# Performance work log

Measured on AMD Instinct MI355X. Metric: run time of the kernel, lower is better.

## Reference

```python
import math
import jax, jax.numpy as jnp
import numpy as np

CHUNK = 32
PROB_FLOOR = 0.02
EPS = 1e-5

def l2norm(x):
    return x * jax.lax.rsqrt(jnp.sum(x * x, -1, keepdims=True) + 1e-6)

def causal_dwconv(x, w):
    # x: (B, L, C), w: (C, K) depthwise causal FIR (left-padded)
    B, L, C = x.shape
    K = w.shape[-1]
    y = jax.lax.conv_general_dilated(jnp.transpose(x, (0, 2, 1)), w[:, None, :], (1,), [(K - 1, 0)], feature_group_count=C)
    return jnp.transpose(y, (0, 2, 1))

def delta_rule_chunkwise(q, k, v, beta, chunk=CHUNK):
    # q,k: (b,h,L,dk)  v: (b,h,L,dv)  beta: (b,h,L)
    b, h, L, dk = q.shape
    dv = v.shape[-1]
    pad = (-L) % chunk
    if pad:
        q = jnp.pad(q, ((0, 0), (0, 0), (0, pad), (0, 0)))
        k = jnp.pad(k, ((0, 0), (0, 0), (0, pad), (0, 0)))
        v = jnp.pad(v, ((0, 0), (0, 0), (0, pad), (0, 0)))
        beta = jnp.pad(beta, ((0, 0), (0, 0), (0, pad)))
    Lp = L + pad
    n = Lp // chunk
    q = l2norm(q)
    k = l2norm(k)
    v = v * beta[..., None]
    kb = k * beta[..., None]
    r = lambda t: t.reshape(b, h, n, chunk, t.shape[-1])
    q, k, v, kb = (r(q), r(k), r(v), r(kb))
    i_ = jnp.arange(chunk)
    strict_lower = (i_[:, None] > i_[None, :]).astype(q.dtype)
    lower_incl = (i_[:, None] >= i_[None, :]).astype(q.dtype)
    inv = -(kb @ jnp.swapaxes(k, -1, -2)) * strict_lower  # (b,h,n,c,c)
    for i in range(1, chunk):  # row-wise forward substitution; chunk is static so unrolled
        inv = inv.at[..., i, :].add(jnp.einsum('...j,...jk->...k', inv[..., i, :], inv))
    inv = inv + jnp.eye(chunk, dtype=q.dtype)
    u = inv @ v   # (b,h,n,c,dv)
    w = inv @ kb  # (b,h,n,c,dk)
    mv = lambda t: jnp.moveaxis(t, 2, 0)  # scan over chunks
    def step(S, xs):
        qi, ki, ui, wi = xs
        attn = (qi @ jnp.swapaxes(ki, -1, -2)) * lower_incl
        ui2 = ui - wi @ S
        oi = qi @ S + attn @ ui2
        return S + jnp.swapaxes(ki, -1, -2) @ ui2, oi
    S0 = jnp.zeros((b, h, dk, dv), q.dtype)
    S, outs = jax.lax.scan(step, S0, (mv(q), mv(k), mv(u), mv(w)))
    out = jnp.moveaxis(outs, 0, 2).reshape(b, h, Lp, dv)[:, :, :L]
    return out, S

def head_stats(x):
    # x: (B,L,H,D) -> (B,L,4): [mean, var, abs-mean, l2] per head, averaged over heads
    mean = x.mean(-1)
    var = ((x - mean[..., None]) ** 2).mean(-1)
    am = jnp.abs(x).mean(-1)
    l2 = jnp.sqrt((x * x).sum(-1))
    return jnp.stack([mean, var, am, l2], -1).mean(2)

def rmsnorm(x, w):
    return x * jax.lax.rsqrt((x * x).mean(-1, keepdims=True) + EPS) * w

def setup_inputs():
    key = jax.random.key(0)
    ks = jax.random.split(key, 20)
    B, L, D, H = 2, 4096, 1024, 4
    dv = D // H
    f32 = jnp.float32
    rn = lambda k, shape, s: (jax.random.normal(k, shape) * s).astype(f32)
    fir = lambda k, shape: rn(k, shape, 0.02).at[..., -1].add(1.0)  # near-identity causal filter
    return {
        'hidden_states': jax.random.normal(ks[0], (B, L, D), f32),
        'Wq': rn(ks[1], (D, D), 0.02), 'Wk': rn(ks[2], (D, D), 0.02), 'Wv': rn(ks[3], (D, D), 0.02),
        'Wb': rn(ks[4], (D, H), 0.02),
        'wq_conv': fir(ks[5], (D, 4)), 'wk_conv': fir(ks[6], (D, 4)), 'wv_conv': fir(ks[7], (D, 4)),
        'fir_long': fir(ks[8], (H, dv, 64)), 'fir_short': fir(ks[9], (H, dv, 5)),
        'Wg1': rn(ks[10], (D + 16, D), 0.02), 'bg1': jnp.zeros((D,), f32),
        'Wg2': rn(ks[11], (D, 4), 0.02), 'bg2': jnp.array([-0.5, -0.5, 1.0, 3.0], f32),
        'logit_temp': jnp.array([math.log(math.expm1(0.7))], f32),
        'conv_res_logit': jnp.full((H,), -1.0, f32),
        'Wres': rn(ks[12], (D, H), 0.02), 'bres': jnp.full((H,), -1.0, f32),
        'Wog1': rn(ks[13], (D + 8, D // 2), 0.02), 'bog1': jnp.zeros((D // 2,), f32),
        'Wog2': rn(ks[14], (D // 2, 1), 0.02), 'bog2': jnp.full((1,), -1.0986122886681098, f32),
        'norm_w': jnp.ones((dv,), f32),
        'Wo': rn(ks[15], (D, D), 0.02),
    }

def reference(hidden_states, Wq, Wk, Wv, Wb, wq_conv, wk_conv, wv_conv, fir_long, fir_short, Wg1, bg1, Wg2, bg2, logit_temp, conv_res_logit, Wres, bres, Wog1, bog1, Wog2, bog2, norm_w, Wo):
    B, L, D = hidden_states.shape
    H = Wb.shape[-1]
    silu = jax.nn.silu
    q_in = silu(causal_dwconv(hidden_states @ Wq, wq_conv))
    k_in = silu(causal_dwconv(hidden_states @ Wk, wk_conv))
    v_in = silu(causal_dwconv(hidden_states @ Wv, wv_conv))
    dk = q_in.shape[-1] // H
    dv = v_in.shape[-1] // H
    q = q_in.reshape(B, L, H, dk)
    k = k_in.reshape(B, L, H, dk)
    v_direct = v_in.reshape(B, L, H, dv)
    beta = jax.nn.sigmoid(hidden_states @ Wb)  # (B,L,H)
    do, S = delta_rule_chunkwise(jnp.transpose(q, (0, 2, 1, 3)), jnp.transpose(k, (0, 2, 1, 3)), jnp.transpose(v_direct, (0, 2, 1, 3)), jnp.transpose(beta, (0, 2, 1)))
    delta_out = jnp.transpose(do, (0, 2, 1, 3))  # (B,L,H,dv)
    local_long = causal_dwconv(v_in, fir_long.reshape(-1, fir_long.shape[-1])).reshape(B, L, H, dv)
    local_short = causal_dwconv(v_in, fir_short.reshape(-1, fir_short.shape[-1])).reshape(B, L, H, dv)
    stats = jnp.concatenate([head_stats(t) for t in (local_short, local_long, delta_out, v_direct)], -1)  # (B,L,16)
    gate_in = jnp.concatenate([hidden_states, stats], -1)
    logits = (jax.nn.gelu(gate_in @ Wg1 + bg1, approximate=False) @ Wg2 + bg2) / jax.nn.softplus(logit_temp)
    p = jax.nn.softmax(logits, -1)
    p = jnp.clip(p, PROB_FLOOR, None)
    p = p / p.sum(-1, keepdims=True)
    pw = p[:, :, None, :]  # (B,L,1,4)
    o = pw[..., 0:1] * local_short + pw[..., 1:2] * local_long + pw[..., 2:3] * delta_out + pw[..., 3:4] * v_direct
    res_gate = jax.nn.sigmoid(hidden_states @ Wres + bres)  # (B,L,H)
    static = jax.nn.sigmoid(conv_res_logit)  # (H,)
    o = o + (static[None, None, :] * res_gate)[..., None] * local_short
    og_stats = jnp.concatenate([head_stats(o), head_stats(v_direct)], -1)  # (B,L,8)
    og_in = jnp.concatenate([hidden_states, og_stats], -1)
    og = jax.nn.sigmoid(jax.nn.gelu(og_in @ Wog1 + bog1, approximate=False) @ Wog2 + bog2)  # (B,L,1)
    o = o * og[:, :, :, None]
    o = rmsnorm(o, norm_w)
    return o.reshape(B, L, -1) @ Wo
```

## Files before the change

### kernel.cpp

```cpp
#include <hip/hip_runtime.h>
#include <math.h>

#define B_ 2
#define L_ 4096
#define D_ 1024
#define H_ 4
#define DH 256
#define CHUNKSZ 32
#define NCH (L_/CHUNKSZ)
#define BL (B_*L_)
#define BLD (B_*L_*D_)

typedef __attribute__((ext_vector_type(8))) short bf16x8;
typedef __attribute__((ext_vector_type(4))) float f32x4;

__device__ __forceinline__ float sigmf(float x) { return 1.f / (1.f + expf(-x)); }
__device__ __forceinline__ float geluf(float x) { return 0.5f * x * (1.f + erff(x * 0.70710678118654752f)); }
__device__ __forceinline__ unsigned short f2bf(float f) {
  unsigned int u = __float_as_uint(f);
  unsigned int r = (u + 0x7FFFu + ((u >> 16) & 1u)) >> 16;
  return (unsigned short)r;
}
__device__ __forceinline__ unsigned int pk2bf(float a, float b) {
  return ((unsigned int)f2bf(b) << 16) | (unsigned int)f2bf(a);
}

__global__ __launch_bounds__(256)
void cvt_bf16(const float* __restrict__ x, unsigned short* __restrict__ y, long n) {
  long i = ((long)blockIdx.x * 256 + threadIdx.x) * 4;
  if (i >= n) return;
  float4 v = *reinterpret_cast<const float4*>(&x[i]);
  ushort4 o;
  o.x = f2bf(v.x); o.y = f2bf(v.y); o.z = f2bf(v.z); o.w = f2bf(v.w);
  *reinterpret_cast<ushort4*>(&y[i]) = o;
}

__global__ __launch_bounds__(256)
void wconv_t(const float* __restrict__ W, unsigned short* __restrict__ Wt, int N) {
  __shared__ float tile[32][33];
  int kb = blockIdx.y * 32, nb = blockIdx.x * 32;
  int tx = threadIdx.x & 31, ty = threadIdx.x >> 5;
  for (int i = 0; i < 32; i += 8)
    tile[ty + i][tx] = W[(long)(kb + ty + i) * N + nb + tx];
  __syncthreads();
  for (int i = 0; i < 32; i += 8)
    Wt[(long)(nb + ty + i) * 1024 + kb + tx] = f2bf(tile[tx][ty + i]);
}

__global__ __launch_bounds__(256)
void gemm_bf16(const unsigned short* __restrict__ A, const unsigned short* __restrict__ Bt,
               float* __restrict__ C, int N) {
  __shared__ unsigned short Al[128 * 32];
  __shared__ unsigned short Bl[128 * 32];
  const int K = 1024;
  int nBn = N >> 7;
  int wgid = blockIdx.x;
  int xcd = wgid & 7;
  int local = wgid >> 3;
  int bm = (xcd * 8 + local / nBn) * 128;
  int bn = (local % nBn) * 128;
  int tid = threadIdx.x;
  int lane = tid & 63, wid = tid >> 6;
  int wr = wid >> 1, wc = wid & 1;
  int l15 = lane & 15, l4 = lane >> 4;
  f32x4 acc[4][4];
#pragma unroll
  for (int i = 0; i < 4; ++i)
#pragma unroll
    for (int j = 0; j < 4; ++j) { acc[i][j].x = 0.f; acc[i][j].y = 0.f; acc[i][j].z = 0.f; acc[i][j].w = 0.f; }
  for (int k0 = 0; k0 < K; k0 += 32) {
    __syncthreads();
#pragma unroll
    for (int i = 0; i < 2; ++i) {
      int idx = tid + i * 256;
      int r = idx >> 2, sl = idx & 3;
      int src = sl ^ ((r >> 1) & 3);
      __builtin_amdgcn_global_load_lds(
          (const __attribute__((address_space(1))) unsigned int*)&A[(long)(bm + r) * K + k0 + src * 8],
          (__attribute__((address_space(3))) unsigned int*)&Al[idx * 8], 16, 0, 0);
      __builtin_amdgcn_global_load_lds(
          (const __attribute__((address_space(1))) unsigned int*)&Bt[(long)(bn + r) * K + k0 + src * 8],
          (__attribute__((address_space(3))) unsigned int*)&Bl[idx * 8], 16, 0, 0);
    }
    __syncthreads();
    bf16x8 af[4], bfr[4];
#pragma unroll
    for (int fi = 0; fi < 4; ++fi) {
      int r = wr * 64 + fi * 16 + l15;
      af[fi] = *reinterpret_cast<const bf16x8*>(&Al[r * 32 + (l4 ^ ((r >> 1) & 3)) * 8]);
    }
#pragma unroll
    for (int fj = 0; fj < 4; ++fj) {
      int r = wc * 64 + fj * 16 + l15;
      bfr[fj] = *reinterpret_cast<const bf16x8*>(&Bl[r * 32 + (l4 ^ ((r >> 1) & 3)) * 8]);
    }
#pragma unroll
    for (int fi = 0; fi < 4; ++fi)
#pragma unroll
      for (int fj = 0; fj < 4; ++fj)
        acc[fi][fj] = __builtin_amdgcn_mfma_f32_16x16x32_bf16(af[fi], bfr[fj], acc[fi][fj], 0, 0, 0);
  }
#pragma unroll
  for (int fi = 0; fi < 4; ++fi) {
    int rb = bm + wr * 64 + fi * 16 + l4 * 4;
#pragma unroll
    for (int fj = 0; fj < 4; ++fj) {
      int cb = bn + wc * 64 + fj * 16 + l15;
#pragma unroll
      for (int j = 0; j < 4; ++j)
        C[(long)(rb + j) * N + cb] = acc[fi][fj][j];
    }
  }
}

#define CTL 128
template<int K>
__global__ __launch_bounds__(256)
void dwconv_tiled(const float* __restrict__ x, const float* __restrict__ w,
                  float* __restrict__ y, int do_silu) {
  __shared__ float tile[(CTL + K - 1) * 64];
  int bid = blockIdx.x;
  int ct = bid & 15;
  int lt = (bid >> 4) & 31;
  int b  = bid >> 9;
  int c0 = ct * 64;
  int l0 = lt * CTL;
  int tid = threadIdx.x;
  const int rows = CTL + K - 1;
  for (int i = tid; i < rows * 16; i += 256) {
    int rr = i >> 4, c4 = i & 15;
    int l = l0 - (K - 1) + rr;
    float4 v = make_float4(0.f, 0.f, 0.f, 0.f);
    if (l >= 0) v = *reinterpret_cast<const float4*>(&x[((long)b * L_ + l) * D_ + c0 + c4 * 4]);
    *reinterpret_cast<float4*>(&tile[rr * 64 + c4 * 4]) = v;
  }
  __syncthreads();
  int c = tid & 63;
  int wv = tid >> 6;
  float wreg[K];
#pragma unroll
  for (int j = 0; j < K; ++j) wreg[j] = w[(long)(c0 + c) * K + j];
#pragma unroll
  for (int g = 0; g < 4; ++g) {
    int lo_base = g * 32 + wv * 8;
    float win[8];
#pragma unroll
    for (int r = 0; r < 8; ++r) win[r] = tile[(lo_base + r) * 64 + c];
    float acc[8] = {0.f, 0.f, 0.f, 0.f, 0.f, 0.f, 0.f, 0.f};
#pragma unroll
    for (int j = 0; j < K; ++j) {
#pragma unroll
      for (int r = 0; r < 8; ++r) acc[r] = fmaf(wreg[j], win[r], acc[r]);
      if (j < K - 1) {
#pragma unroll
        for (int r = 0; r < 7; ++r) win[r] = win[r + 1];
        win[7] = tile[(lo_base + j + 8) * 64 + c];
      }
    }
#pragma unroll
    for (int r = 0; r < 8; ++r) {
      float v = acc[r];
      if (do_silu) v = v * sigmf(v);
      y[((long)b * L_ + l0 + lo_base + r) * D_ + c0 + c] = v;
    }
  }
}

__global__ __launch_bounds__(256)
void l2norm_wave(float* __restrict__ x) {
  long row = (long)blockIdx.x * 4 + (threadIdx.x >> 6);
  int lane = threadIdx.x & 63;
  float4 v = *reinterpret_cast<const float4*>(&x[row * 256 + lane * 4]);
  float q = v.x * v.x + v.y * v.y + v.z * v.z + v.w * v.w;
#pragma unroll
  for (int st = 32; st > 0; st >>= 1) q += __shfl_xor(q, st);
  float inv = rsqrtf(q + 1e-6f);
  v.x *= inv; v.y *= inv; v.z *= inv; v.w *= inv;
  *reinterpret_cast<float4*>(&x[row * 256 + lane * 4]) = v;
}

__global__ __launch_bounds__(256)
void beta_res_gemv(const float* __restrict__ hs, const float* __restrict__ Wb,
                   const float* __restrict__ Wres, const float* __restrict__ bres,
                   float* __restrict__ beta, float* __restrict__ resg) {
  long m = blockIdx.x;
  int n = threadIdx.x >> 6, lane = threadIdx.x & 63;
  float ab = 0.f, ar = 0.f;
  for (int k0 = lane * 4; k0 < 1024; k0 += 256) {
    float4 x = *reinterpret_cast<const float4*>(&hs[m * 1024 + k0]);
    ab += x.x * Wb[(k0 + 0) * 4 + n] + x.y * Wb[(k0 + 1) * 4 + n]
        + x.z * Wb[(k0 + 2) * 4 + n] + x.w * Wb[(k0 + 3) * 4 + n];
    ar += x.x * Wres[(k0 + 0) * 4 + n] + x.y * Wres[(k0 + 1) * 4 + n]
        + x.z * Wres[(k0 + 2) * 4 + n] + x.w * Wres[(k0 + 3) * 4 + n];
  }
#pragma unroll
  for (int st = 32; st > 0; st >>= 1) { ab += __shfl_xor(ab, st); ar += __shfl_xor(ar, st); }
  if (lane == 0) {
    beta[m * 4 + n] = sigmf(ab);
    resg[m * 4 + n] = sigmf(ar + bres[n]);
  }
}

__global__ __launch_bounds__(256)
void chunk_uw(const float* __restrict__ qn, const float* __restrict__ kn,
              const float* __restrict__ v, const float* __restrict__ beta,
              float* __restrict__ u,
              unsigned short* __restrict__ q_bf, unsigned short* __restrict__ w_bf,
              unsigned short* __restrict__ kT_bf, unsigned short* __restrict__ at_bf) {
  __shared__ float skT[256][33];
  __shared__ float sinv[32][33];
  __shared__ float sbeta[32];
  int blk = blockIdx.x;
  int ci = blk % NCH;
  int bh = blk / NCH;
  int h = bh % H_;
  int b = bh / H_;
  long base = ((long)b * L_ + (long)ci * CHUNKSZ) * D_ + h * DH;
  long brow = (long)b * L_ + (long)ci * CHUNKSZ;
  long obase = (long)blk * 8192;
  int tid = threadIdx.x;
  for (int i = tid; i < 32 * 256; i += 256) {
    int r = i >> 8, c = i & 255;
    skT[c][r] = kn[base + (long)r * D_ + c];
  }
  if (tid < 32) sbeta[tid] = beta[(brow + tid) * H_ + h];
  __syncthreads();
  for (int i = tid; i < 8192; i += 256)
    kT_bf[obase + i] = f2bf(skT[i >> 5][i & 31]);
  for (int i = tid; i < 8192; i += 256)
    q_bf[obase + i] = f2bf(qn[base + (long)(i >> 8) * D_ + (i & 255)]);
  int j = tid & 31, i0 = tid >> 5;
  for (int r = 0; r < 4; ++r) {
    int i = i0 + (r << 3);
    float acc = 0.f;
    for (int d = 0; d < 256; ++d) acc += skT[d][i] * skT[d][j];
    sinv[i][j] = (i > j) ? -acc * sbeta[i] : 0.f;
  }
  __syncthreads();
  for (int i = 1; i < 32; ++i) {
    float val = 0.f;
    if (tid < 32) {
      for (int t = 0; t < i; ++t) val += sinv[i][t] * sinv[t][tid];
    }
    __syncthreads();
    if (tid < 32) sinv[i][tid] += val;
    __syncthreads();
  }
  if (tid < 32) sinv[tid][tid] += 1.f;
  long abase = (long)blk * 1024;
  for (int r = 0; r < 4; ++r) {
    int i = i0 + (r << 3);
    const float* qrow = qn + base + (long)i * D_;
    float acc = 0.f;
    for (int d = 0; d < 256; ++d) acc += qrow[d] * skT[d][j];
    at_bf[abase + i * 32 + j] = f2bf((i >= j) ? acc : 0.f);
  }
  __syncthreads();
  int c = tid;
  float vt[32], kt[32];
#pragma unroll
  for (int t = 0; t < 32; ++t) {
    vt[t] = v[base + t * D_ + c] * sbeta[t];
    kt[t] = skT[c][t] * sbeta[t];
  }
#pragma unroll
  for (int i2 = 0; i2 < 32; ++i2) {
    float au = 0.f, aw = 0.f;
#pragma unroll
    for (int t = 0; t <= i2; ++t) {
      float f = sinv[i2][t];
      au += f * vt[t];
      aw += f * kt[t];
    }
    u[base + i2 * D_ + c] = au;
    w_bf[obase + i2 * 256 + c] = f2bf(aw);
  }
}

__global__ __launch_bounds__(64, 1)
void delta_scan(const unsigned short* __restrict__ qb, const unsigned short* __restrict__ wbf,
                const unsigned short* __restrict__ ktb, const unsigned short* __restrict__ atb,
                const float* __restrict__ u, float* __restrict__ out) {
  __shared__ unsigned short sB[16 * 264];
  __shared__ unsigned short su2[16 * 40];
  int blk = blockIdx.x;
  int bh = blk & 7, cg = blk >> 3;
  int h = bh & 3, b = bh >> 2;
  int lane = threadIdx.x;
  int l15 = lane & 15, l4 = lane >> 4;
  int colw = cg * 16;

  f32x4 zero4; zero4.x = 0.f; zero4.y = 0.f; zero4.z = 0.f; zero4.w = 0.f;
  f32x4 acc[16];
#pragma unroll
  for (int t = 0; t < 16; ++t) acc[t] = zero4;

  uint4 wf[2][8];
  float ru[2][4];
  uint4 qf[2][8];
  uint4 kfa[8], kfb[8];
  uint4 af[2];

#define LOAD_W(CI) do {                                                          \
    long o8_ = ((long)bh * NCH + (CI)) * 8192;                                   \
    _Pragma("unroll")                                                            \
    for (int m_ = 0; m_ < 2; ++m_)                                               \
      _Pragma("unroll")                                                          \
      for (int kc_ = 0; kc_ < 8; ++kc_)                                          \
        wf[m_][kc_] = *reinterpret_cast<const uint4*>(                           \
            &wbf[o8_ + (16 * m_ + l15) * 256 + kc_ * 32 + l4 * 8]);              \
  } while (0)

#define LOAD_U(CI) do {                                                          \
    long ub_ = ((long)b * L_ + (long)(CI) * CHUNKSZ) * D_ + h * DH + colw;       \
    _Pragma("unroll")                                                            \
    for (int m_ = 0; m_ < 2; ++m_)                                               \
      _Pragma("unroll")                                                          \
      for (int r_ = 0; r_ < 4; ++r_)                                             \
        ru[m_][r_] = u[ub_ + (long)(16 * m_ + 4 * l4 + r_) * D_ + l15];          \
  } while (0)

#define LOAD_Q(CI) do {                                                          \
    long o8_ = ((long)bh * NCH + (CI)) * 8192;                                   \
    _Pragma("unroll")                                                            \
    for (int m_ = 0; m_ < 2; ++m_)                                               \
      _Pragma("unroll")                                                          \
      for (int kc_ = 0; kc_ < 8; ++kc_)                                          \
        qf[m_][kc_] = *reinterpret_cast<const uint4*>(                           \
            &qb[o8_ + (16 * m_ + l15) * 256 + kc_ * 32 + l4 * 8]);               \
  } while (0)

#define LOAD_KA(CI) do {                                                         \
    long o8_ = ((long)bh * NCH + (CI)) * 8192;                                   \
    _Pragma("unroll")                                                            \
    for (int dt_ = 0; dt_ < 8; ++dt_)                                            \
      kfa[dt_] = *reinterpret_cast<const uint4*>(                                \
          &ktb[o8_ + (16 * dt_ + l15) * 32 + l4 * 8]);                           \
  } while (0)

#define LOAD_KB(CI) do {                                                         \
    long o8_ = ((long)bh * NCH + (CI)) * 8192;                                   \
    _Pragma("unroll")                                                            \
    for (int dt_ = 0; dt_ < 8; ++dt_)                                            \
      kfb[dt_] = *reinterpret_cast<const uint4*>(                                \
          &ktb[o8_ + (16 * (dt_ + 8) + l15) * 32 + l4 * 8]);                     \
  } while (0)

#define LOAD_A(CI) do {                                                          \
    long oa_ = ((long)bh * NCH + (CI)) * 1024;                                   \
    _Pragma("unroll")                                                            \
    for (int m_ = 0; m_ < 2; ++m_)                                               \
      af[m_] = *reinterpret_cast<const uint4*>(                                  \
          &atb[oa_ + (16 * m_ + l15) * 32 + l4 * 8]);                            \
  } while (0)

#define SCAN_BODY(CI, PF) do {                                                   \
    long ub = ((long)b * L_ + (long)(CI) * CHUNKSZ) * D_ + h * DH + colw;        \
    _Pragma("unroll")                                                            \
    for (int dt = 0; dt < 16; ++dt) {                                            \
      uint2 pv;                                                                  \
      pv.x = pk2bf(acc[dt].x, acc[dt].y);                                        \
      pv.y = pk2bf(acc[dt].z, acc[dt].w);                                        \
      *reinterpret_cast<uint2*>(&sB[l15 * 264 + dt * 16 + l4 * 4]) = pv;         \
    }                                                                            \
    bf16x8 sf[8];                                                                \
    _Pragma("unroll")                                                            \
    for (int kc = 0; kc < 8; ++kc)                                               \
      sf[kc] = *reinterpret_cast<const bf16x8*>(&sB[l15 * 264 + kc * 32 + l4 * 8]); \
    f32x4 wa[2][2];                                                              \
    wa[0][0] = zero4; wa[0][1] = zero4; wa[1][0] = zero4; wa[1][1] = zero4;      \
    _Pragma("unroll")                                                            \
    for (int kc = 0; kc < 8; ++kc) {                                             \
      _Pragma("unroll")                                                          \
      for (int m = 0; m < 2; ++m)                                                \
        wa[m][kc & 1] = __builtin_amdgcn_mfma_f32_16x16x32_bf16(                 \
            *reinterpret_cast<bf16x8*>(&wf[m][kc]), sf[kc], wa[m][kc & 1], 0, 0, 0); \
    }                                                                            \
    if (PF) LOAD_W((CI) + 1);                                                    \
    _Pragma("unroll")                                                            \
    for (int m = 0; m < 2; ++m) {                                                \
      f32x4 wsum = wa[m][0] + wa[m][1];                                          \
      uint2 pv;                                                                  \
      pv.x = pk2bf(ru[m][0] - wsum.x, ru[m][1] - wsum.y);                        \
      pv.y = pk2bf(ru[m][2] - wsum.z, ru[m][3] - wsum.w);                        \
      *reinterpret_cast<uint2*>(&su2[l15 * 40 + m * 16 + l4 * 4]) = pv;          \
    }                                                                            \
    if (PF) LOAD_U((CI) + 1);                                                    \
    bf16x8 u2f = *reinterpret_cast<const bf16x8*>(&su2[l15 * 40 + l4 * 8]);      \
    _Pragma("unroll")                                                            \
    for (int dt = 0; dt < 8; ++dt)                                               \
      acc[dt] = __builtin_amdgcn_mfma_f32_16x16x32_bf16(                         \
          *reinterpret_cast<bf16x8*>(&kfa[dt]), u2f, acc[dt], 0, 0, 0);          \
    if (PF) LOAD_KA((CI) + 1);                                                   \
    _Pragma("unroll")                                                            \
    for (int dt = 0; dt < 8; ++dt)                                               \
      acc[dt + 8] = __builtin_amdgcn_mfma_f32_16x16x32_bf16(                     \
          *reinterpret_cast<bf16x8*>(&kfb[dt]), u2f, acc[dt + 8], 0, 0, 0);      \
    if (PF) LOAD_KB((CI) + 1);                                                   \
    f32x4 qa[2][2];                                                              \
    qa[0][0] = zero4; qa[0][1] = zero4; qa[1][0] = zero4; qa[1][1] = zero4;      \
    _Pragma("unroll")                                                            \
    for (int kc = 0; kc < 8; ++kc) {                                             \
      _Pragma("unroll")                                                          \
      for (int m = 0; m < 2; ++m)                                                \
        qa[m][kc & 1] = __builtin_amdgcn_mfma_f32_16x16x32_bf16(                 \
            *reinterpret_cast<bf16x8*>(&qf[m][kc]), sf[kc], qa[m][kc & 1], 0, 0, 0); \
    }                                                                            \
    if (PF) LOAD_Q((CI) + 1);                                                    \
    _Pragma("unroll")                                                            \
    for (int m = 0; m < 2; ++m) {                                                \
      f32x4 qacc = qa[m][0] + qa[m][1];                                          \
      f32x4 dv = __builtin_amdgcn_mfma_f32_16x16x32_bf16(                        \
          *reinterpret_cast<bf16x8*>(&af[m]), u2f, qacc, 0, 0, 0);               \
      _Pragma("unroll")                                                          \
      for (int r = 0; r < 4; ++r)                                                \
        out[ub + (long)(16 * m + 4 * l4 + r) * D_ + l15] = dv[r];                \
    }                                                                            \
    if (PF) LOAD_A((CI) + 1);                                                    \
  } while (0)

  LOAD_W(0); LOAD_U(0); LOAD_Q(0); LOAD_KA(0); LOAD_KB(0); LOAD_A(0);

  for (int ci = 0; ci < NCH - 1; ++ci) {
    SCAN_BODY(ci, 1);
  }
  SCAN_BODY(NCH - 1, 0);

#undef LOAD_W
#undef LOAD_U
#undef LOAD_Q
#undef LOAD_KA
#undef LOAD_KB
#undef LOAD_A
#undef SCAN_BODY
}

__global__ __launch_bounds__(256)
void head_stats4(const float* __restrict__ t0, const float* __restrict__ t1,
                 const float* __restrict__ t2, const float* __restrict__ t3,
                 float* __restrict__ outp) {
  long bl = blockIdx.x;
  int w = threadIdx.x >> 6, lane = threadIdx.x & 63;
  const float* x = (w == 0) ? t0 : (w == 1) ? t1 : (w == 2) ? t2 : t3;
  float m = 0.f, vv = 0.f, am = 0.f, l2 = 0.f;
#pragma unroll
  for (int h = 0; h < 4; ++h) {
    float4 v = *reinterpret_cast<const float4*>(&x[bl * 1024 + h * 256 + lane * 4]);
    float s = v.x + v.y + v.z + v.w;
    float q = v.x * v.x + v.y * v.y + v.z * v.z + v.w * v.w;
    float a = fabsf(v.x) + fabsf(v.y) + fabsf(v.z) + fabsf(v.w);
#pragma unroll
    for (int st = 32; st > 0; st >>= 1) {
      s += __shfl_xor(s, st); q += __shfl_xor(q, st); a += __shfl_xor(a, st);
    }
    float mean = s * (1.f / 256.f);
    m += mean;
    vv += q * (1.f / 256.f) - mean * mean;
    am += a * (1.f / 256.f);
    l2 += sqrtf(q);
  }
  if (lane == 0) {
    float* o = outp + bl * 16 + w * 4;
    o[0] = m * 0.25f; o[1] = vv * 0.25f; o[2] = am * 0.25f; o[3] = l2 * 0.25f;
  }
}

__global__ __launch_bounds__(256)
void gate_fused(const float* __restrict__ g, const float* __restrict__ stats,
                const float* __restrict__ Wg1t, const float* __restrict__ bg1,
                const float* __restrict__ Wg2, const float* __restrict__ bg2,
                const float* __restrict__ temp_in, float* __restrict__ p) {
  __shared__ float red[4][4];
  long m = blockIdx.x;
  int tid = threadIdx.x;
  int c0 = tid * 4;
  float4 gv = *reinterpret_cast<const float4*>(&g[m * 1024 + c0]);
  float st[16];
#pragma unroll
  for (int k = 0; k < 16; ++k) st[k] = stats[m * 16 + k];
  float la[4] = {0.f, 0.f, 0.f, 0.f};
  float gvv[4] = {gv.x, gv.y, gv.z, gv.w};
#pragma unroll
  for (int j = 0; j < 4; ++j) {
    int c = c0 + j;
    float s = gvv[j] + bg1[c];
#pragma unroll
    for (int k = 0; k < 16; ++k) s += st[k] * Wg1t[(long)k * 1024 + c];
    float ge = geluf(s);
#pragma unroll
    for (int n = 0; n < 4; ++n) la[n] += ge * Wg2[c * 4 + n];
  }
#pragma unroll
  for (int stp = 32; stp > 0; stp >>= 1)
#pragma unroll
    for (int n = 0; n < 4; ++n) la[n] += __shfl_xor(la[n], stp);
  int w = tid >> 6;
  if ((tid & 63) == 0) {
#pragma unroll
    for (int n = 0; n < 4; ++n) red[w][n] = la[n];
  }
  __syncthreads();
  if (tid == 0) {
    float temp = log1pf(expf(temp_in[0]));
    float l[4];
#pragma unroll
    for (int n = 0; n < 4; ++n)
      l[n] = (red[0][n] + red[1][n] + red[2][n] + red[3][n] + bg2[n]) / temp;
    float mx = fmaxf(fmaxf(l[0], l[1]), fmaxf(l[2], l[3]));
    float e[4], s = 0.f;
#pragma unroll
    for (int n = 0; n < 4; ++n) { e[n] = expf(l[n] - mx); s += e[n]; }
    float s2 = 0.f;
#pragma unroll
    for (int n = 0; n < 4; ++n) { e[n] = fmaxf(e[n] / s, 0.02f); s2 += e[n]; }
#pragma unroll
    for (int n = 0; n < 4; ++n) p[m * 4 + n] = e[n] / s2;
  }
}

__global__ __launch_bounds__(256)
void combine_ogstats(const float* __restrict__ ls, const float* __restrict__ ll,
                     const float* __restrict__ dd, const float* __restrict__ vd,
                     const float* __restrict__ p, const float* __restrict__ resg,
                     const float* __restrict__ crl, float* __restrict__ o,
                     float* __restrict__ og8) {
  __shared__ float part[4][8];
  long bl = blockIdx.x;
  int h = threadIdx.x >> 6, lane = threadIdx.x & 63;
  long base = bl * 1024 + h * 256 + lane * 4;
  float4 lsv = *reinterpret_cast<const float4*>(&ls[base]);
  float4 llv = *reinterpret_cast<const float4*>(&ll[base]);
  float4 ddv = *reinterpret_cast<const float4*>(&dd[base]);
  float4 vdv = *reinterpret_cast<const float4*>(&vd[base]);
  float p0 = p[bl * 4 + 0], p1 = p[bl * 4 + 1], p2 = p[bl * 4 + 2], p3 = p[bl * 4 + 3];
  float sg = sigmf(crl[h]) * resg[bl * 4 + h];
  float c0 = p0 + sg;
  float4 ov;
  ov.x = c0 * lsv.x + p1 * llv.x + p2 * ddv.x + p3 * vdv.x;
  ov.y = c0 * lsv.y + p1 * llv.y + p2 * ddv.y + p3 * vdv.y;
  ov.z = c0 * lsv.z + p1 * llv.z + p2 * ddv.z + p3 * vdv.z;
  ov.w = c0 * lsv.w + p1 * llv.w + p2 * ddv.w + p3 * vdv.w;
  *reinterpret_cast<float4*>(&o[base]) = ov;
  float s = ov.x + ov.y + ov.z + ov.w;
  float q = ov.x * ov.x + ov.y * ov.y + ov.z * ov.z + ov.w * ov.w;
  float a = fabsf(ov.x) + fabsf(ov.y) + fabsf(ov.z) + fabsf(ov.w);
  float sv = vdv.x + vdv.y + vdv.z + vdv.w;
  float qv = vdv.x * vdv.x + vdv.y * vdv.y + vdv.z * vdv.z + vdv.w * vdv.w;
  float av = fabsf(vdv.x) + fabsf(vdv.y) + fabsf(vdv.z) + fabsf(vdv.w);
#pragma unroll
  for (int st = 32; st > 0; st >>= 1) {
    s += __shfl_xor(s, st); q += __shfl_xor(q, st); a += __shfl_xor(a, st);
    sv += __shfl_xor(sv, st); qv += __shfl_xor(qv, st); av += __shfl_xor(av, st);
  }
  if (lane == 0) {
    float mo = s * (1.f / 256.f), mv = sv * (1.f / 256.f);
    part[h][0] = mo; part[h][1] = q * (1.f / 256.f) - mo * mo;
    part[h][2] = a * (1.f / 256.f); part[h][3] = sqrtf(q);
    part[h][4] = mv; part[h][5] = qv * (1.f / 256.f) - mv * mv;
    part[h][6] = av * (1.f / 256.f); part[h][7] = sqrtf(qv);
  }
  __syncthreads();
  if (threadIdx.x < 8) {
    int t = threadIdx.x;
    og8[bl * 8 + t] = 0.25f * (part[0][t] + part[1][t] + part[2][t] + part[3][t]);
  }
}

__global__ __launch_bounds__(256)
void og_gate_fused(const float* __restrict__ g, const float* __restrict__ og8,
                   const float* __restrict__ Wog1t, const float* __restrict__ bog1,
                   const float* __restrict__ Wog2, const float* __restrict__ bog2,
                   float* __restrict__ ogv) {
  __shared__ float red[4];
  long m = blockIdx.x;
  int tid = threadIdx.x;
  int c0 = tid * 2;
  float2 gv = *reinterpret_cast<const float2*>(&g[m * 512 + c0]);
  float st[8];
#pragma unroll
  for (int k = 0; k < 8; ++k) st[k] = og8[m * 8 + k];
  float a = 0.f;
  float gvv[2] = {gv.x, gv.y};
#pragma unroll
  for (int j = 0; j < 2; ++j) {
    int c = c0 + j;
    float s = gvv[j] + bog1[c];
#pragma unroll
    for (int k = 0; k < 8; ++k) s += st[k] * Wog1t[(long)k * 512 + c];
    a += geluf(s) * Wog2[c];
  }
#pragma unroll
  for (int stp = 32; stp > 0; stp >>= 1) a += __shfl_xor(a, stp);
  int w = tid >> 6;
  if ((tid & 63) == 0) red[w] = a;
  __syncthreads();
  if (tid == 0) ogv[m] = sigmf(red[0] + red[1] + red[2] + red[3] + bog2[0]);
}

__global__ __launch_bounds__(256)
void scale_rmsnorm_bf16(const float* __restrict__ o, const float* __restrict__ og,
                        const float* __restrict__ nw, unsigned short* __restrict__ xb) {
  long row = (long)blockIdx.x * 4 + (threadIdx.x >> 6);
  long bl = row >> 2;
  int lane = threadIdx.x & 63;
  float g = og[bl];
  float4 v = *reinterpret_cast<const float4*>(&o[row * 256 + lane * 4]);
  v.x *= g; v.y *= g; v.z *= g; v.w *= g;
  float q = v.x * v.x + v.y * v.y + v.z * v.z + v.w * v.w;
#pragma unroll
  for (int st = 32; st > 0; st >>= 1) q += __shfl_xor(q, st);
  float scale = rsqrtf(q * (1.f / 256.f) + 1e-5f);
  float4 w4 = *reinterpret_cast<const float4*>(&nw[lane * 4]);
  ushort4 r;
  r.x = f2bf(v.x * scale * w4.x);
  r.y = f2bf(v.y * scale * w4.y);
  r.z = f2bf(v.z * scale * w4.z);
  r.w = f2bf(v.w * scale * w4.w);
  *reinterpret_cast<ushort4*>(&xb[row * 256 + lane * 4]) = r;
}

extern "C" void kernel_launch(void* const* d_in, const int* in_sizes, int n_in,
                              void* d_out, int out_size, void* d_ws, size_t ws_size,
                              hipStream_t stream) {
  const float* hs       = (const float*)d_in[0];
  const float* Wq       = (const float*)d_in[1];
  const float* Wk       = (const float*)d_in[2];
  const float* Wv       = (const float*)d_in[3];
  const float* Wb       = (const float*)d_in[4];
  const float* wq_conv  = (const float*)d_in[5];
  const float* wk_conv  = (const float*)d_in[6];
  const float* wv_conv  = (const float*)d_in[7];
  const float* fir_long = (const float*)d_in[8];
  const float* fir_short= (const float*)d_in[9];
  const float* Wg1      = (const float*)d_in[10];
  const float* bg1      = (const float*)d_in[11];
  const float* Wg2      = (const float*)d_in[12];
  const float* bg2      = (const float*)d_in[13];
  const float* logit_temp     = (const float*)d_in[14];
  const float* conv_res_logit = (const float*)d_in[15];
  const float* Wres     = (const float*)d_in[16];
  const float* bres     = (const float*)d_in[17];
  const float* Wog1     = (const float*)d_in[18];
  const float* bog1     = (const float*)d_in[19];
  const float* Wog2     = (const float*)d_in[20];
  const float* bog2     = (const float*)d_in[21];
  const float* norm_w   = (const float*)d_in[22];
  const float* Wo       = (const float*)d_in[23];
  float* out = (float*)d_out;
  float* ws = (float*)d_ws;

  float* b0 = ws;
  float* b1 = ws + 1L * BLD;
  float* b2 = ws + 2L * BLD;
  float* b3 = ws + 3L * BLD;
  float* b4 = ws + 4L * BLD;
  float* sm = ws + 5L * BLD;
  float* beta    = sm;
  float* resg    = beta + BL * H_;
  float* stats16 = resg + BL * H_;
  float* og8     = stats16 + BL * 16;
  float* logits  = og8 + BL * 8;
  float* pbuf    = logits + BL * 4;
  float* ogv     = pbuf + BL * 4;
  unsigned short* q_bfg  = (unsigned short*)(ogv + BL);
  unsigned short* kT_bfg = q_bfg + (long)BLD;
  unsigned short* at_bfg = kT_bfg + (long)BLD;
  unsigned short* hsb  = at_bfg + 1024L * 1024;
  unsigned short* wtq  = hsb + (long)BLD;
  unsigned short* wtk  = wtq + 1024L * 1024;
  unsigned short* wtv  = wtk + 1024L * 1024;
  unsigned short* wtg1 = wtv + 1024L * 1024;
  unsigned short* wto  = wtg1 + 1024L * 1024;
  unsigned short* wtog1= wto + 1024L * 1024;
  unsigned short* w_bfg = (unsigned short*)b4;
  unsigned short* xb    = q_bfg;

  size_t needed = (5L * BLD + BL * 41) * 4
                + (3L * BLD + 1024L * 1024 + 5L * 1024 * 1024 + 512L * 1024) * 2;
  if (ws_size < needed) return;

  dim3 blk(256);
  wconv_t<<<dim3(32, 32), blk, 0, stream>>>(Wq, wtq, 1024);
  wconv_t<<<dim3(32, 32), blk, 0, stream>>>(Wk, wtk, 1024);
  wconv_t<<<dim3(32, 32), blk, 0, stream>>>(Wv, wtv, 1024);
  wconv_t<<<dim3(32, 32), blk, 0, stream>>>(Wg1, wtg1, 1024);
  wconv_t<<<dim3(32, 32), blk, 0, stream>>>(Wo, wto, 1024);
  wconv_t<<<dim3(16, 32), blk, 0, stream>>>(Wog1, wtog1, 512);
  cvt_bf16<<<BLD / 1024, blk, 0, stream>>>(hs, hsb, BLD);
  gemm_bf16<<<512, blk, 0, stream>>>(hsb, wtq, b0, 1024);
  gemm_bf16<<<512, blk, 0, stream>>>(hsb, wtk, b1, 1024);
  gemm_bf16<<<512, blk, 0, stream>>>(hsb, wtv, b2, 1024);
  dwconv_tiled<4><<<1024, blk, 0, stream>>>(b0, wq_conv, b3, 1);
  dwconv_tiled<4><<<1024, blk, 0, stream>>>(b1, wk_conv, b0, 1);
  dwconv_tiled<4><<<1024, blk, 0, stream>>>(b2, wv_conv, b1, 1);
  beta_res_gemv<<<BL, blk, 0, stream>>>(hs, Wb, Wres, bres, beta, resg);
  l2norm_wave<<<BL * H_ / 4, blk, 0, stream>>>(b3);
  l2norm_wave<<<BL * H_ / 4, blk, 0, stream>>>(b0);
  chunk_uw<<<B_ * H_ * NCH, blk, 0, stream>>>(b3, b0, b1, beta, b2, q_bfg, w_bfg, kT_bfg, at_bfg);
  delta_scan<<<128, dim3(64), 0, stream>>>(q_bfg, w_bfg, kT_bfg, at_bfg, b2, b2);
  dwconv_tiled<64><<<1024, blk, 0, stream>>>(b1, fir_long, b3, 0);
  dwconv_tiled<5><<<1024, blk, 0, stream>>>(b1, fir_short, b4, 0);
  head_stats4<<<BL, blk, 0, stream>>>(b4, b3, b2, b1, stats16);
  gemm_bf16<<<512, blk, 0, stream>>>(hsb, wtg1, b0, 1024);
  gate_fused<<<BL, blk, 0, stream>>>(b0, stats16, Wg1 + 1024L * 1024, bg1, Wg2, bg2, logit_temp, pbuf);
  combine_ogstats<<<BL, blk, 0, stream>>>(b4, b3, b2, b1, pbuf, resg, conv_res_logit, b0, og8);
  gemm_bf16<<<256, blk, 0, stream>>>(hsb, wtog1, b2, 512);
  og_gate_fused<<<BL, blk, 0, stream>>>(b2, og8, Wog1 + 1024L * 512, bog1, Wog2, bog2, ogv);
  scale_rmsnorm_bf16<<<BL * H_ / 4, blk, 0, stream>>>(b0, ogv, norm_w, xb);
  gemm_bf16<<<512, blk, 0, stream>>>(xb, wto, out, 1024);
}
```

Baseline: 933.8 us.

## Batch QKV and gate/og GEMMs, fuse weight conversion, cvt+beta, and l2norms

Result: faster. 806.6 us (-13.6%).

```diff
diff --git a/kernel.cpp b/kernel.cpp
--- a/kernel.cpp
+++ b/kernel.cpp
@@ -26,25 +26,212 @@
 }
 
 __global__ __launch_bounds__(256)
-void cvt_bf16(const float* __restrict__ x, unsigned short* __restrict__ y, long n) {
-  long i = ((long)blockIdx.x * 256 + threadIdx.x) * 4;
-  if (i >= n) return;
-  float4 v = *reinterpret_cast<const float4*>(&x[i]);
-  ushort4 o;
-  o.x = f2bf(v.x); o.y = f2bf(v.y); o.z = f2bf(v.z); o.w = f2bf(v.w);
-  *reinterpret_cast<ushort4*>(&y[i]) = o;
-}
-
-__global__ __launch_bounds__(256)
-void wconv_t(const float* __restrict__ W, unsigned short* __restrict__ Wt, int N) {
+void wconv_all(const float* __restrict__ Wq, const float* __restrict__ Wk,
+               const float* __restrict__ Wv, const float* __restrict__ Wg1,
+               const float* __restrict__ Wog1, const float* __restrict__ Wo,
+               unsigned short* __restrict__ wtq, unsigned short* __restrict__ wtk,
+               unsigned short* __restrict__ wtv, unsigned short* __restrict__ wtg1,
+               unsigned short* __restrict__ wtog1, unsigned short* __restrict__ wto) {
   __shared__ float tile[32][33];
-  int kb = blockIdx.y * 32, nb = blockIdx.x * 32;
+  int bid = blockIdx.x;
+  const float* W; unsigned short* Wt; int N; int rem;
+  if (bid < 5120) {
+    int widx = bid >> 10; rem = bid & 1023; N = 1024;
+    switch (widx) {
+      case 0: W = Wq; Wt = wtq; break;
+      case 1: W = Wk; Wt = wtk; break;
+      case 2: W = Wv; Wt = wtv; break;
+      case 3: W = Wg1; Wt = wtg1; break;
+      default: W = Wo; Wt = wto; break;
+    }
+  } else { rem = bid - 5120; N = 512; W = Wog1; Wt = wtog1; }
+  int nT = N >> 5;
+  int nb = (rem % nT) * 32, kb = (rem / nT) * 32;
   int tx = threadIdx.x & 31, ty = threadIdx.x >> 5;
   for (int i = 0; i < 32; i += 8)
     tile[ty + i][tx] = W[(long)(kb + ty + i) * N + nb + tx];
   __syncthreads();
   for (int i = 0; i < 32; i += 8)
     Wt[(long)(nb + ty + i) * 1024 + kb + tx] = f2bf(tile[tx][ty + i]);
+}
+
+__global__ __launch_bounds__(256)
+void cvt_beta(const float* __restrict__ hs, unsigned short* __restrict__ hsb,
+              const float* __restrict__ Wb, const float* __restrict__ Wres,
+              const float* __restrict__ bres,
+              float* __restrict__ beta, float* __restrict__ resg) {
+  __shared__ float red[4][8];
+  long m = blockIdx.x;
+  int tid = threadIdx.x;
+  int k0 = tid * 4;
+  float4 x = *reinterpret_cast<const float4*>(&hs[m * 1024 + k0]);
+  ushort4 o;
+  o.x = f2bf(x.x); o.y = f2bf(x.y); o.z = f2bf(x.z); o.w = f2bf(x.w);
+  *reinterpret_cast<ushort4*>(&hsb[m * 1024 + k0]) = o;
+  float xr[4] = {x.x, x.y, x.z, x.w};
+  float ab[4] = {0.f, 0.f, 0.f, 0.f}, ar[4] = {0.f, 0.f, 0.f, 0.f};
+#pragma unroll
+  for (int j = 0; j < 4; ++j) {
+    float4 wb = *reinterpret_cast<const float4*>(&Wb[(long)(k0 + j) * 4]);
+    float4 wr = *reinterpret_cast<const float4*>(&Wres[(long)(k0 + j) * 4]);
+    ab[0] = fmaf(xr[j], wb.x, ab[0]); ab[1] = fmaf(xr[j], wb.y, ab[1]);
+    ab[2] = fmaf(xr[j], wb.z, ab[2]); ab[3] = fmaf(xr[j], wb.w, ab[3]);
+    ar[0] = fmaf(xr[j], wr.x, ar[0]); ar[1] = fmaf(xr[j], wr.y, ar[1]);
+    ar[2] = fmaf(xr[j], wr.z, ar[2]); ar[3] = fmaf(xr[j], wr.w, ar[3]);
+  }
+#pragma unroll
+  for (int st = 32; st > 0; st >>= 1) {
+#pragma unroll
+    for (int n = 0; n < 4; ++n) { ab[n] += __shfl_xor(ab[n], st); ar[n] += __shfl_xor(ar[n], st); }
+  }
+  int w = tid >> 6;
+  if ((tid & 63) == 0) {
+#pragma unroll
+    for (int n = 0; n < 4; ++n) { red[w][n] = ab[n]; red[w][n + 4] = ar[n]; }
+  }
+  __syncthreads();
+  if (tid < 8) {
+    float s = red[0][tid] + red[1][tid] + red[2][tid] + red[3][tid];
+    if (tid < 4) beta[m * 4 + tid] = sigmf(s);
+    else resg[m * 4 + tid - 4] = sigmf(s + bres[tid - 4]);
+  }
+}
+
+__global__ __launch_bounds__(256)
+void gemm_qkv(const unsigned short* __restrict__ A, const unsigned short* __restrict__ Bt,
+              float* __restrict__ C0) {
+  __shared__ unsigned short Al[128 * 32];
+  __shared__ unsigned short Bl[128 * 32];
+  const int K = 1024;
+  const int nBn = 24;
+  int wgid = blockIdx.x;
+  int xcd = wgid & 7;
+  int local = wgid >> 3;
+  int bm = (xcd * 8 + local / nBn) * 128;
+  int bn = (local % nBn) * 128;
+  float* Cd = C0 + (long)(bn >> 10) * BLD;
+  int cbn = bn & 1023;
+  int tid = threadIdx.x;
+  int lane = tid & 63, wid = tid >> 6;
+  int wr = wid >> 1, wc = wid & 1;
+  int l15 = lane & 15, l4 = lane >> 4;
+  f32x4 acc[4][4];
+#pragma unroll
+  for (int i = 0; i < 4; ++i)
+#pragma unroll
+    for (int j = 0; j < 4; ++j) { acc[i][j].x = 0.f; acc[i][j].y = 0.f; acc[i][j].z = 0.f; acc[i][j].w = 0.f; }
+  for (int k0 = 0; k0 < K; k0 += 32) {
+    __syncthreads();
+#pragma unroll
+    for (int i = 0; i < 2; ++i) {
+      int idx = tid + i * 256;
+      int r = idx >> 2, sl = idx & 3;
+      int src = sl ^ ((r >> 1) & 3);
+      __builtin_amdgcn_global_load_lds(
+          (const __attribute__((address_space(1))) unsigned int*)&A[(long)(bm + r) * K + k0 + src * 8],
+          (__attribute__((address_space(3))) unsigned int*)&Al[idx * 8], 16, 0, 0);
+      __builtin_amdgcn_global_load_lds(
+          (const __attribute__((address_space(1))) unsigned int*)&Bt[(long)(bn + r) * K + k0 + src * 8],
+          (__attribute__((address_space(3))) unsigned int*)&Bl[idx * 8], 16, 0, 0);
+    }
+    __syncthreads();
+    bf16x8 af[4], bfr[4];
+#pragma unroll
+    for (int fi = 0; fi < 4; ++fi) {
+      int r = wr * 64 + fi * 16 + l15;
+      af[fi] = *reinterpret_cast<const bf16x8*>(&Al[r * 32 + (l4 ^ ((r >> 1) & 3)) * 8]);
+    }
+#pragma unroll
+    for (int fj = 0; fj < 4; ++fj) {
+      int r = wc * 64 + fj * 16 + l15;
+      bfr[fj] = *reinterpret_cast<const bf16x8*>(&Bl[r * 32 + (l4 ^ ((r >> 1) & 3)) * 8]);
+    }
+#pragma unroll
+    for (int fi = 0; fi < 4; ++fi)
+#pragma unroll
+      for (int fj = 0; fj < 4; ++fj)
+        acc[fi][fj] = __builtin_amdgcn_mfma_f32_16x16x32_bf16(af[fi], bfr[fj], acc[fi][fj], 0, 0, 0);
+  }
+#pragma unroll
+  for (int fi = 0; fi < 4; ++fi) {
+    int rb = bm + wr * 64 + fi * 16 + l4 * 4;
+#pragma unroll
+    for (int fj = 0; fj < 4; ++fj) {
+      int cb = cbn + wc * 64 + fj * 16 + l15;
+#pragma unroll
+      for (int j = 0; j < 4; ++j)
+        Cd[(long)(rb + j) * 1024 + cb] = acc[fi][fj][j];
+    }
+  }
+}
+
+__global__ __launch_bounds__(256)
+void gemm_gateog(const unsigned short* __restrict__ A, const unsigned short* __restrict__ Bt,
+                 float* __restrict__ Cg, float* __restrict__ Cog) {
+  __shared__ unsigned short Al[128 * 32];
+  __shared__ unsigned short Bl[128 * 32];
+  const int K = 1024;
+  const int nBn = 12;
+  int wgid = blockIdx.x;
+  int xcd = wgid & 7;
+  int local = wgid >> 3;
+  int bm = (xcd * 8 + local / nBn) * 128;
+  int bn = (local % nBn) * 128;
+  float* Cd; int stride, cbn;
+  if (bn < 1024) { Cd = Cg; stride = 1024; cbn = bn; }
+  else { Cd = Cog; stride = 512; cbn = bn - 1024; }
+  int tid = threadIdx.x;
+  int lane = tid & 63, wid = tid >> 6;
+  int wr = wid >> 1, wc = wid & 1;
+  int l15 = lane & 15, l4 = lane >> 4;
+  f32x4 acc[4][4];
+#pragma unroll
+  for (int i = 0; i < 4; ++i)
+#pragma unroll
+    for (int j = 0; j < 4; ++j) { acc[i][j].x = 0.f; acc[i][j].y = 0.f; acc[i][j].z = 0.f; acc[i][j].w = 0.f; }
+  for (int k0 = 0; k0 < K; k0 += 32) {
+    __syncthreads();
+#pragma unroll
+    for (int i = 0; i < 2; ++i) {
+      int idx = tid + i * 256;
+      int r = idx >> 2, sl = idx & 3;
+      int src = sl ^ ((r >> 1) & 3);
+      __builtin_amdgcn_global_load_lds(
+          (const __attribute__((address_space(1))) unsigned int*)&A[(long)(bm + r) * K + k0 + src * 8],
+          (__attribute__((address_space(3))) unsigned int*)&Al[idx * 8], 16, 0, 0);
+      __builtin_amdgcn_global_load_lds(
+          (const __attribute__((address_space(1))) unsigned int*)&Bt[(long)(bn + r) * K + k0 + src * 8],
+          (__attribute__((address_space(3))) unsigned int*)&Bl[idx * 8], 16, 0, 0);
+    }
+    __syncthreads();
+    bf16x8 af[4], bfr[4];
+#pragma unroll
+    for (int fi = 0; fi < 4; ++fi) {
+      int r = wr * 64 + fi * 16 + l15;
+      af[fi] = *reinterpret_cast<const bf16x8*>(&Al[r * 32 + (l4 ^ ((r >> 1) & 3)) * 8]);
+    }
+#pragma unroll
+    for (int fj = 0; fj < 4; ++fj) {
+      int r = wc * 64 + fj * 16 + l15;
+      bfr[fj] = *reinterpret_cast<const bf16x8*>(&Bl[r * 32 + (l4 ^ ((r >> 1) & 3)) * 8]);
+    }
+#pragma unroll
+    for (int fi = 0; fi < 4; ++fi)
+#pragma unroll
+      for (int fj = 0; fj < 4; ++fj)
+        acc[fi][fj] = __builtin_amdgcn_mfma_f32_16x16x32_bf16(af[fi], bfr[fj], acc[fi][fj], 0, 0, 0);
+  }
+#pragma unroll
+  for (int fi = 0; fi < 4; ++fi) {
+    int rb = bm + wr * 64 + fi * 16 + l4 * 4;
+#pragma unroll
+    for (int fj = 0; fj < 4; ++fj) {
+      int cb = cbn + wc * 64 + fj * 16 + l15;
+#pragma unroll
+      for (int j = 0; j < 4; ++j)
+        Cd[(long)(rb + j) * stride + cb] = acc[fi][fj][j];
+    }
+  }
 }
 
 __global__ __launch_bounds__(256)
@@ -167,8 +354,12 @@
 }
 
 __global__ __launch_bounds__(256)
-void l2norm_wave(float* __restrict__ x) {
-  long row = (long)blockIdx.x * 4 + (threadIdx.x >> 6);
+void l2norm_wave2(float* __restrict__ x0, float* __restrict__ x1) {
+  int bid = blockIdx.x;
+  const int half = BL * H_ / 4;
+  float* x = (bid < half) ? x0 : x1;
+  int lb = (bid < half) ? bid : bid - half;
+  long row = (long)lb * 4 + (threadIdx.x >> 6);
   int lane = threadIdx.x & 63;
   float4 v = *reinterpret_cast<const float4*>(&x[row * 256 + lane * 4]);
   float q = v.x * v.x + v.y * v.y + v.z * v.z + v.w * v.w;
@@ -177,28 +368,6 @@
   float inv = rsqrtf(q + 1e-6f);
   v.x *= inv; v.y *= inv; v.z *= inv; v.w *= inv;
   *reinterpret_cast<float4*>(&x[row * 256 + lane * 4]) = v;
-}
-
-__global__ __launch_bounds__(256)
-void beta_res_gemv(const float* __restrict__ hs, const float* __restrict__ Wb,
-                   const float* __restrict__ Wres, const float* __restrict__ bres,
-                   float* __restrict__ beta, float* __restrict__ resg) {
-  long m = blockIdx.x;
-  int n = threadIdx.x >> 6, lane = threadIdx.x & 63;
-  float ab = 0.f, ar = 0.f;
-  for (int k0 = lane * 4; k0 < 1024; k0 += 256) {
-    float4 x = *reinterpret_cast<const float4*>(&hs[m * 1024 + k0]);
-    ab += x.x * Wb[(k0 + 0) * 4 + n] + x.y * Wb[(k0 + 1) * 4 + n]
-        + x.z * Wb[(k0 + 2) * 4 + n] + x.w * Wb[(k0 + 3) * 4 + n];
-    ar += x.x * Wres[(k0 + 0) * 4 + n] + x.y * Wres[(k0 + 1) * 4 + n]
-        + x.z * Wres[(k0 + 2) * 4 + n] + x.w * Wres[(k0 + 3) * 4 + n];
-  }
-#pragma unroll
-  for (int st = 32; st > 0; st >>= 1) { ab += __shfl_xor(ab, st); ar += __shfl_xor(ar, st); }
-  if (lane == 0) {
-    beta[m * 4 + n] = sigmf(ab);
-    resg[m * 4 + n] = sigmf(ar + bres[n]);
-  }
 }
 
 __global__ __launch_bounds__(256)
@@ -670,42 +839,33 @@
   unsigned short* wtk  = wtq + 1024L * 1024;
   unsigned short* wtv  = wtk + 1024L * 1024;
   unsigned short* wtg1 = wtv + 1024L * 1024;
-  unsigned short* wto  = wtg1 + 1024L * 1024;
-  unsigned short* wtog1= wto + 1024L * 1024;
+  unsigned short* wtog1= wtg1 + 1024L * 1024;
+  unsigned short* wto  = wtog1 + 512L * 1024;
   unsigned short* w_bfg = (unsigned short*)b4;
   unsigned short* xb    = q_bfg;
+  float* ogh = (float*)q_bfg;
 
   size_t needed = (5L * BLD + BL * 41) * 4
                 + (3L * BLD + 1024L * 1024 + 5L * 1024 * 1024 + 512L * 1024) * 2;
   if (ws_size < needed) return;
 
   dim3 blk(256);
-  wconv_t<<<dim3(32, 32), blk, 0, stream>>>(Wq, wtq, 1024);
-  wconv_t<<<dim3(32, 32), blk, 0, stream>>>(Wk, wtk, 1024);
-  wconv_t<<<dim3(32, 32), blk, 0, stream>>>(Wv, wtv, 1024);
-  wconv_t<<<dim3(32, 32), blk, 0, stream>>>(Wg1, wtg1, 1024);
-  wconv_t<<<dim3(32, 32), blk, 0, stream>>>(Wo, wto, 1024);
-  wconv_t<<<dim3(16, 32), blk, 0, stream>>>(Wog1, wtog1, 512);
-  cvt_bf16<<<BLD / 1024, blk, 0, stream>>>(hs, hsb, BLD);
-  gemm_bf16<<<512, blk, 0, stream>>>(hsb, wtq, b0, 1024);
-  gemm_bf16<<<512, blk, 0, stream>>>(hsb, wtk, b1, 1024);
-  gemm_bf16<<<512, blk, 0, stream>>>(hsb, wtv, b2, 1024);
+  wconv_all<<<5632, blk, 0, stream>>>(Wq, Wk, Wv, Wg1, Wog1, Wo, wtq, wtk, wtv, wtg1, wtog1, wto);
+  cvt_beta<<<BL, blk, 0, stream>>>(hs, hsb, Wb, Wres, bres, beta, resg);
+  gemm_qkv<<<1536, blk, 0, stream>>>(hsb, wtq, b0);
   dwconv_tiled<4><<<1024, blk, 0, stream>>>(b0, wq_conv, b3, 1);
   dwconv_tiled<4><<<1024, blk, 0, stream>>>(b1, wk_conv, b0, 1);
   dwconv_tiled<4><<<1024, blk, 0, stream>>>(b2, wv_conv, b1, 1);
-  beta_res_gemv<<<BL, blk, 0, stream>>>(hs, Wb, Wres, bres, beta, resg);
-  l2norm_wave<<<BL * H_ / 4, blk, 0, stream>>>(b3);
-  l2norm_wave<<<BL * H_ / 4, blk, 0, stream>>>(b0);
+  l2norm_wave2<<<2 * BL * H_ / 4, blk, 0, stream>>>(b3, b0);
   chunk_uw<<<B_ * H_ * NCH, blk, 0, stream>>>(b3, b0, b1, beta, b2, q_bfg, w_bfg, kT_bfg, at_bfg);
   delta_scan<<<128, dim3(64), 0, stream>>>(q_bfg, w_bfg, kT_bfg, at_bfg, b2, b2);
   dwconv_tiled<64><<<1024, blk, 0, stream>>>(b1, fir_long, b3, 0);
   dwconv_tiled<5><<<1024, blk, 0, stream>>>(b1, fir_short, b4, 0);
   head_stats4<<<BL, blk, 0, stream>>>(b4, b3, b2, b1, stats16);
-  gemm_bf16<<<512, blk, 0, stream>>>(hsb, wtg1, b0, 1024);
+  gemm_gateog<<<768, blk, 0, stream>>>(hsb, wtg1, b0, ogh);
   gate_fused<<<BL, blk, 0, stream>>>(b0, stats16, Wg1 + 1024L * 1024, bg1, Wg2, bg2, logit_temp, pbuf);
   combine_ogstats<<<BL, blk, 0, stream>>>(b4, b3, b2, b1, pbuf, resg, conv_res_logit, b0, og8);
-  gemm_bf16<<<256, blk, 0, stream>>>(hsb, wtog1, b2, 512);
-  og_gate_fused<<<BL, blk, 0, stream>>>(b2, og8, Wog1 + 1024L * 512, bog1, Wog2, bog2, ogv);
+  og_gate_fused<<<BL, blk, 0, stream>>>(ogh, og8, Wog1 + 1024L * 512, bog1, Wog2, bog2, ogv);
   scale_rmsnorm_bf16<<<BL * H_ / 4, blk, 0, stream>>>(b0, ogv, norm_w, xb);
   gemm_bf16<<<512, blk, 0, stream>>>(xb, wto, out, 1024);
 }
```
